# Performance work log

Hardware: AMD Instinct MI355X
Metric: run time of the kernel (lower is better)

Reference implementation:

```python
import jax, jax.numpy as jnp
import numpy as np

N = 5000          # nodes (pool_ratios = [2000/5000, 0.5])
KS = (2000, 1000, 500)  # top-k sizes per level, depth=3
H = 128           # inter_dim
IN = 3            # xyz
OUT = 6890        # SMPL template vertices
E = 80000


def _gcn(adj, x, W, b):
    # GCNConv: add self-loops (weight 1), symmetric normalization
    n = adj.shape[0]
    A = adj + jnp.eye(n, dtype=adj.dtype)
    dinv = jax.lax.rsqrt(A.sum(axis=1))
    Ahat = dinv[:, None] * A * dinv[None, :]
    return Ahat @ (x @ W) + b


def _augment(adj):
    # GraphUNet.augment_adj: remove self loops, add self loops, A @ A, remove self loops
    n = adj.shape[0]
    eye = jnp.eye(n, dtype=adj.dtype)
    A = adj * (1.0 - eye) + eye
    A2 = A @ A
    return A2 * (1.0 - eye)


def _pool(x, adj, w, k):
    # TopKPooling: score = tanh(x.w / ||w||), keep top-k, scale kept features by score
    score = jnp.tanh((x @ w) / jnp.linalg.norm(w))
    sc, perm = jax.lax.top_k(score, k)
    x = x[perm] * sc[:, None]
    adj = adj[perm][:, perm]
    return x, adj, perm


def reference(pos, edge_index, Wd0, bd0, Wd1, bd1, Wd2, bd2, Wd3, bd3,
              pw0, pw1, pw2, Wu0, bu0, Wu1, bu1, Wu2, bu2,
              W1, b1, W2, b2, W3, b3):
    # eval mode: dropout_adj(p=0.1, training=False) is identity
    adj = jnp.zeros((N, N), pos.dtype).at[edge_index[0], edge_index[1]].add(1.0)

    x = jax.nn.relu(_gcn(adj, pos, Wd0, bd0))
    xs, adjs, perms = [x], [adj], []
    Wds = [(Wd1, bd1), (Wd2, bd2), (Wd3, bd3)]
    pws = [pw0, pw1, pw2]

    adj_cur = adj
    for i in range(3):
        a = _augment(adj_cur)
        x, adj_cur, perm = _pool(x, a, pws[i], KS[i])
        Wi, bi = Wds[i]
        x = jax.nn.relu(_gcn(adj_cur, x, Wi, bi))
        if i < 2:
            xs.append(x)
            adjs.append(adj_cur)
        perms.append(perm)

    Wus = [(Wu0, bu0), (Wu1, bu1), (Wu2, bu2)]
    for i in range(3):
        j = 2 - i
        res = xs[j]
        up = jnp.zeros_like(res).at[perms[j]].set(x)  # unpool: scatter back
        x = res + up                                   # sum_res=True
        Wi, bi = Wus[i]
        x = _gcn(adjs[j], x, Wi, bi)
        if i < 2:
            x = jax.nn.relu(x)

    x = x @ W1 + b1
    x = jax.nn.relu(x) @ W2 + b2
    x = x @ W3 + b3
    return jax.nn.log_softmax(x, axis=1)


def _glorot(k, shape):
    return (jax.random.normal(k, shape) * np.sqrt(2.0 / (shape[0] + shape[1]))).astype(jnp.float32)


def setup_inputs() -> dict:
    key = jax.random.key(0)
    ks = jax.random.split(key, 16)
    inp = {
        'pos': jax.random.normal(ks[0], (N, IN), dtype=jnp.float32),
        'edge_index': jax.random.randint(ks[1], (2, E), 0, N, dtype=jnp.int64),
        'Wd0': _glorot(ks[2], (IN, H)), 'bd0': jnp.zeros((H,), jnp.float32),
        'Wd1': _glorot(ks[3], (H, H)), 'bd1': jnp.zeros((H,), jnp.float32),
        'Wd2': _glorot(ks[4], (H, H)), 'bd2': jnp.zeros((H,), jnp.float32),
        'Wd3': _glorot(ks[5], (H, H)), 'bd3': jnp.zeros((H,), jnp.float32),
        'pw0': jax.random.normal(ks[6], (H,), dtype=jnp.float32) / np.sqrt(H),
        'pw1': jax.random.normal(ks[7], (H,), dtype=jnp.float32) / np.sqrt(H),
        'pw2': jax.random.normal(ks[8], (H,), dtype=jnp.float32) / np.sqrt(H),
        'Wu0': _glorot(ks[9], (H, H)), 'bu0': jnp.zeros((H,), jnp.float32),
        'Wu1': _glorot(ks[10], (H, H)), 'bu1': jnp.zeros((H,), jnp.float32),
        'Wu2': _glorot(ks[11], (H, H)), 'bu2': jnp.zeros((H,), jnp.float32),
        'W1': _glorot(ks[12], (H, H)), 'b1': jnp.zeros((H,), jnp.float32),
        'W2': _glorot(ks[13], (H, H)), 'b2': jnp.zeros((H,), jnp.float32),
        'W3': _glorot(ks[14], (H, OUT)), 'b3': jnp.zeros((OUT,), jnp.float32),
    }
    return inp
```

## Files before the change

### kernel.cpp

```cpp
#include <hip/hip_runtime.h>
#include <cmath>

#define CDIV(a,b) (((a)+(b)-1)/(b))

using u16 = unsigned short;
using short8 = __attribute__((ext_vector_type(8))) short;
using f32x4 = __attribute__((ext_vector_type(4))) float;

__device__ __forceinline__ u16 f2b(float v) {
    union { float f; unsigned u; } x; x.f = v;
    unsigned r = x.u + 0x7fffu + ((x.u >> 16) & 1u);
    return (u16)(r >> 16);
}
__device__ __forceinline__ float b2f(u16 h) {
    union { unsigned u; float f; } x; x.u = ((unsigned)h) << 16;
    return x.f;
}

#if defined(__has_builtin)
#if __has_builtin(__builtin_amdgcn_global_load_lds)
#define HAS_GLL 1
#endif
#endif
#ifndef HAS_GLL
#define HAS_GLL 0
#endif

__device__ __forceinline__ void g2l(const u16* g, uint4* l) {
#if HAS_GLL
    __builtin_amdgcn_global_load_lds((const __attribute__((address_space(1))) void*)g,
                                     (__attribute__((address_space(3))) void*)l, 16, 0, 0);
#else
    *l = *(const uint4*)g;
#endif
}


__global__ void csr_cnt_k(const int* __restrict__ ei, int E, int* __restrict__ rowcnt) {
    int e = blockIdx.x * 256 + threadIdx.x;
    if (e < E) atomicAdd(&rowcnt[ei[e]], 1);
}

__global__ __launch_bounds__(1024) void prefix_k(const int* __restrict__ cnt, int* __restrict__ ptr, int n) {
    __shared__ int buf[5120];
    for (int i = threadIdx.x; i < 5120; i += 1024) buf[i] = (i < n) ? cnt[i] : 0;
    __syncthreads();
    for (int d = 1; d < 5120; d <<= 1) {
        int vals[5];
#pragma unroll
        for (int c = 0; c < 5; ++c) {
            int i = threadIdx.x + c * 1024;
            vals[c] = (i >= d) ? buf[i - d] : 0;
        }
        __syncthreads();
#pragma unroll
        for (int c = 0; c < 5; ++c) {
            int i = threadIdx.x + c * 1024;
            buf[i] += vals[c];
        }
        __syncthreads();
    }
    for (int i = threadIdx.x; i <= n; i += 1024) ptr[i] = (i == 0) ? 0 : buf[i - 1];
}

__global__ void csr_fill_k(const int* __restrict__ ei, int E, const int* __restrict__ rowptr,
                           int* __restrict__ fill, int* __restrict__ cols) {
    int e = blockIdx.x * 256 + threadIdx.x;
    if (e < E) {
        int u = ei[e];
        int p = rowptr[u] + atomicAdd(&fill[u], 1);
        cols[p] = ei[E + e];
    }
}

__global__ void sortrows_k(const int* __restrict__ rowptr, int* __restrict__ cols, int n) {
    int i = blockIdx.x * 256 + threadIdx.x;
    if (i >= n) return;
    int s = rowptr[i], e = rowptr[i + 1];
    for (int p = s + 1; p < e; ++p) {
        int v = cols[p];
        int q = p - 1;
        while (q >= s && cols[q] > v) { cols[q + 1] = cols[q]; --q; }
        cols[q + 1] = v;
    }
}

__global__ void dinv_from_cnt_k(const int* __restrict__ cnt, float* __restrict__ dinv, int n) {
    int i = blockIdx.x * 256 + threadIdx.x;
    if (i < n) dinv[i] = rsqrtf((float)cnt[i] + 1.0f);
}

__global__ __launch_bounds__(128) void spmm_gcn_k(const int* __restrict__ rowptr, const int* __restrict__ cols,
                                                  const float* __restrict__ dinv, const float* __restrict__ xw,
                                                  const float* __restrict__ bias, float* __restrict__ y, int relu) {
    int i = blockIdx.x, f = threadIdx.x;
    int s = rowptr[i], e = rowptr[i + 1];
    float acc = 0.f;
    for (int p = s; p < e; ++p) {
        int d = cols[p];
        acc += dinv[d] * xw[(size_t)d * 128 + f];
    }
    float di = dinv[i];
    float v = di * acc + di * di * xw[(size_t)i * 128 + f] + bias[f];
    y[(size_t)i * 128 + f] = relu ? fmaxf(v, 0.f) : v;
}


__global__ void inv_k(const int* __restrict__ perm, int k, int* __restrict__ inv) {
    int r = blockIdx.x * 256 + threadIdx.x;
    if (r < k) inv[perm[r]] = r;
}

__global__ __launch_bounds__(256) void spgemm_k(const int* __restrict__ perm, const int* __restrict__ rowptr,
                                                const int* __restrict__ cols, const int* __restrict__ inv,
                                                int* __restrict__ A2, int ldo) {
    __shared__ int nb[256];
    __shared__ int degs;
    int a = blockIdx.x;
    int pa = perm[a];
    int s = rowptr[pa], epos = rowptr[pa + 1];
    int d = epos - s;
    if (threadIdx.x == 0) degs = d > 256 ? 256 : d;
    if (threadIdx.x < d && threadIdx.x < 256) nb[threadIdx.x] = cols[s + threadIdx.x];
    __syncthreads();
    int* rowA2 = A2 + (size_t)a * ldo;
    for (int p = s + threadIdx.x; p < epos; p += 256) {
        int c = cols[p];
        if (c != pa) {
            int b = inv[c];
            if (b >= 0) atomicAdd(&rowA2[b], 2);
        }
    }
    int dd = degs;
    for (int j = 0; j < dd; ++j) {
        int kk = nb[j];
        if (kk == pa) continue;
        int s2 = rowptr[kk], e2 = rowptr[kk + 1];
        for (int p = s2 + threadIdx.x; p < e2; p += 256) {
            int pb = cols[p];
            if (pb != kk) {
                int b = inv[pb];
                if (b >= 0) atomicAdd(&rowA2[b], 1);
            }
        }
    }
}

__global__ void conv_spg_k(const int* __restrict__ A2, int kNew, int Mp, u16* __restrict__ out) {
    int r = blockIdx.x;
    for (int j = threadIdx.x; j < Mp; j += 256) {
        int v = 0;
        if (r < kNew && j < kNew && j != r) v = A2[(size_t)r * Mp + j];
        out[(size_t)r * Mp + j] = f2b((float)v);
    }
}


__global__ void rowsum_dinv_b_k(const u16* __restrict__ adjb, int ld, int n, float* __restrict__ dinv) {
    int i = blockIdx.x;
    __shared__ float red[256];
    const u16* row = adjb + (size_t)i * ld;
    float s = 0.f;
    for (int j = threadIdx.x; j < n; j += 256) s += b2f(row[j]);
    red[threadIdx.x] = s; __syncthreads();
    for (int w = 128; w > 0; w >>= 1) {
        if (threadIdx.x < w) red[threadIdx.x] += red[threadIdx.x + w];
        __syncthreads();
    }
    if (threadIdx.x == 0) dinv[i] = rsqrtf(red[0] + 1.0f);
}

__global__ void transpose_b_k(const u16* __restrict__ in, u16* __restrict__ out, int n) {
    __shared__ u16 t[64][65];
    int i0 = blockIdx.y * 64, j0 = blockIdx.x * 64;
    for (int e = threadIdx.x; e < 4096; e += 256) {
        int r = e >> 6, c = e & 63;
        t[r][c] = in[(size_t)(i0 + r) * n + j0 + c];
    }
    __syncthreads();
    for (int e = threadIdx.x; e < 4096; e += 256) {
        int r = e >> 6, c = e & 63;
        out[(size_t)(j0 + r) * n + i0 + c] = t[c][r];
    }
}


template<int SA, int SB>
__global__ __launch_bounds__(256) void mm_nt(const u16* __restrict__ A0, const u16* __restrict__ A1,
                                             const u16* __restrict__ B0, const u16* __restrict__ B1,
                                             float* __restrict__ C, const float* __restrict__ cbias,
                                             int M, int N, int lda, int ldb, int ldc,
                                             int kPerZ, int Kpad, size_t cstride) {
    __shared__ uint4 lds_t[(2 + SA + SB) * 512];
    uint4* Ab  = lds_t;
    uint4* A1b = lds_t + (SA ? 512 : 0);
    uint4* Bb  = lds_t + (1 + SA) * 512;
    uint4* B1b = Bb + (SB ? 512 : 0);

    int tid = threadIdx.x;

    int nx = gridDim.x, nxy = nx * gridDim.y;
    int bx = blockIdx.x, by = blockIdx.y;
    if ((nxy & 7) == 0) {
        int flat = by * nx + bx;
        int nf = (flat & 7) * (nxy >> 3) + (flat >> 3);
        bx = nf % nx; by = nf / nx;
    }
    int row0 = by * 128, col0 = bx * 128;

    int kbeg = blockIdx.z * kPerZ;
    int kend = min(kbeg + kPerZ, Kpad);
    C += (size_t)blockIdx.z * cstride;

    int wave = tid >> 6, lane = tid & 63;
    int wr = (wave >> 1) * 64, wc = (wave & 1) * 64;
    int lrow = lane & 15, kg = lane >> 4;

    int tS0 = tid, tS1 = tid + 256;
    int R0 = ((tS0 >> 6) << 4) | (tS0 & 15), kc0 = (tS0 >> 4) & 3;
    int R1 = ((tS1 >> 6) << 4) | (tS1 & 15), kc1 = (tS1 >> 4) & 3;

    const u16* aP0 = A0 + (size_t)(row0 + R0) * lda + kbeg + kc0 * 8;
    const u16* aP1 = A0 + (size_t)(row0 + R1) * lda + kbeg + kc1 * 8;
    const u16* bP0 = B0 + (size_t)(col0 + R0) * ldb + kbeg + kc0 * 8;
    const u16* bP1 = B0 + (size_t)(col0 + R1) * ldb + kbeg + kc1 * 8;
    const u16* a1P0 = SA ? (A1 + (size_t)(row0 + R0) * lda + kbeg + kc0 * 8) : nullptr;
    const u16* a1P1 = SA ? (A1 + (size_t)(row0 + R1) * lda + kbeg + kc1 * 8) : nullptr;
    const u16* b1P0 = SB ? (B1 + (size_t)(col0 + R0) * ldb + kbeg + kc0 * 8) : nullptr;
    const u16* b1P1 = SB ? (B1 + (size_t)(col0 + R1) * ldb + kbeg + kc1 * 8) : nullptr;

    f32x4 acc[4][4] = {};

    for (int k0 = kbeg; k0 < kend; k0 += 32) {
        __syncthreads();
        g2l(aP0, Ab + tS0);
        g2l(aP1, Ab + tS1);
        if constexpr (SA) { g2l(a1P0, A1b + tS0); g2l(a1P1, A1b + tS1); }
        g2l(bP0, Bb + tS0);
        g2l(bP1, Bb + tS1);
        if constexpr (SB) { g2l(b1P0, B1b + tS0); g2l(b1P1, B1b + tS1); }
        __syncthreads();

        const short8* Ap  = (const short8*)Ab;
        const short8* A1p = (const short8*)A1b;
        const short8* Bp  = (const short8*)Bb;
        const short8* B1p = (const short8*)B1b;

        short8 a[4], a1[4], b[4], b1[4];
#pragma unroll
        for (int m = 0; m < 4; ++m) {
            int idx = (((wr >> 4) + m) << 6) | (kg << 4) | lrow;
            a[m] = Ap[idx];
            if constexpr (SA) a1[m] = A1p[idx];
        }
#pragma unroll
        for (int n = 0; n < 4; ++n) {
            int idx = (((wc >> 4) + n) << 6) | (kg << 4) | lrow;
            b[n] = Bp[idx];
            if constexpr (SB) b1[n] = B1p[idx];
        }
#pragma unroll
        for (int m = 0; m < 4; ++m)
#pragma unroll
            for (int n = 0; n < 4; ++n) {
                acc[m][n] = __builtin_amdgcn_mfma_f32_16x16x32_bf16(a[m], b[n], acc[m][n], 0, 0, 0);
                if constexpr (SA) acc[m][n] = __builtin_amdgcn_mfma_f32_16x16x32_bf16(a1[m], b[n], acc[m][n], 0, 0, 0);
                if constexpr (SB) acc[m][n] = __builtin_amdgcn_mfma_f32_16x16x32_bf16(a[m], b1[n], acc[m][n], 0, 0, 0);
            }

        aP0 += 32; aP1 += 32; bP0 += 32; bP1 += 32;
        if constexpr (SA) { a1P0 += 32; a1P1 += 32; }
        if constexpr (SB) { b1P0 += 32; b1P1 += 32; }
    }

#pragma unroll
    for (int m = 0; m < 4; ++m) {
        int rm = row0 + wr + m * 16 + kg * 4;
#pragma unroll
        for (int n = 0; n < 4; ++n) {
            int cc = col0 + wc + n * 16 + lrow;
            if (cc >= N) continue;
            float badd = cbias ? cbias[cc] : 0.f;
#pragma unroll
            for (int i = 0; i < 4; ++i) {
                int r = rm + i;
                if (r < M) C[(size_t)r * ldc + cc] = acc[m][n][i] + badd;
            }
        }
    }
}


__global__ __launch_bounds__(256) void gemm64(const float* __restrict__ A, const float* __restrict__ B,
                                              float* __restrict__ C,
                                              int M, int N, int K, int lda, int ldb, int ldc,
                                              const float* __restrict__ bias, int relu) {
    __shared__ float As[16][65];
    __shared__ float Bs[16][65];
    int tid = threadIdx.x;
    int trow = tid / 16, tcol = tid % 16;
    int row0 = blockIdx.y * 64 + trow * 4;
    int col0 = blockIdx.x * 64 + tcol * 4;
    float acc[4][4] = {};
    int am = tid >> 2;
    int ak = (tid & 3) * 4;
    int bk = tid >> 4;
    int bn = (tid & 15) * 4;
    for (int k0 = 0; k0 < K; k0 += 16) {
        int gm = blockIdx.y * 64 + am;
#pragma unroll
        for (int u = 0; u < 4; ++u) {
            int gk = k0 + ak + u;
            As[ak + u][am] = (gm < M && gk < K) ? A[(size_t)gm * lda + gk] : 0.f;
        }
        int gbk = k0 + bk;
#pragma unroll
        for (int u = 0; u < 4; ++u) {
            int gn = blockIdx.x * 64 + bn + u;
            Bs[bk][bn + u] = (gbk < K && gn < N) ? B[(size_t)gbk * ldb + gn] : 0.f;
        }
        __syncthreads();
#pragma unroll
        for (int kk = 0; kk < 16; ++kk) {
            float a[4], b[4];
#pragma unroll
            for (int i = 0; i < 4; ++i) a[i] = As[kk][trow * 4 + i];
#pragma unroll
            for (int j = 0; j < 4; ++j) b[j] = Bs[kk][tcol * 4 + j];
#pragma unroll
            for (int i = 0; i < 4; ++i)
#pragma unroll
                for (int j = 0; j < 4; ++j) acc[i][j] += a[i] * b[j];
        }
        __syncthreads();
    }
#pragma unroll
    for (int i = 0; i < 4; ++i) {
        int r = row0 + i;
        if (r >= M) continue;
#pragma unroll
        for (int j = 0; j < 4; ++j) {
            int c = col0 + j;
            if (c < N) {
                float v = acc[i][j] + (bias ? bias[c] : 0.f);
                if (relu) v = fmaxf(v, 0.f);
                C[(size_t)r * ldc + c] = v;
            }
        }
    }
}


__global__ void scale_split_k(const float* __restrict__ xw, const float* __restrict__ dinv,
                              u16* __restrict__ zhT, u16* __restrict__ zlT, int M, int ldz) {
    __shared__ float t[32][33];
    int i0 = blockIdx.x * 32, f0 = blockIdx.y * 32;
#pragma unroll
    for (int it = 0; it < 4; ++it) {
        int r = it * 8 + (threadIdx.x >> 5);
        int c = threadIdx.x & 31;
        int i = i0 + r;
        t[r][c] = (i < M) ? dinv[i] * xw[(size_t)i * 128 + f0 + c] : 0.f;
    }
    __syncthreads();
#pragma unroll
    for (int it = 0; it < 4; ++it) {
        int r = it * 8 + (threadIdx.x >> 5);
        int c = threadIdx.x & 31;
        int f = f0 + r, i = i0 + c;
        float v = t[c][r];
        u16 h = f2b(v);
        zhT[(size_t)f * ldz + i] = h;
        zlT[(size_t)f * ldz + i] = f2b(v - b2f(h));
    }
}

__global__ void reduce_gcn_post_k(const float* __restrict__ part, int Z, int Mp,
                                  const float* __restrict__ xw, const float* __restrict__ dinv,
                                  const float* __restrict__ bias, float* __restrict__ y, int relu) {
    int i = blockIdx.x, f = threadIdx.x;
    size_t idx = (size_t)i * 128 + f;
    float s = 0.f;
    for (int z = 0; z < Z; ++z) s += part[(size_t)z * Mp * 128 + idx];
    float di = dinv[i];
    float v = di * s + di * di * xw[idx] + bias[f];
    y[idx] = relu ? fmaxf(v, 0.f) : v;
}


__global__ void score_k(const float* __restrict__ x, const float* __restrict__ pw,
                        float* __restrict__ score) {
    int i = blockIdx.x;
    __shared__ float red[128], red2[128];
    float p = pw[threadIdx.x];
    red[threadIdx.x]  = x[(size_t)i * 128 + threadIdx.x] * p;
    red2[threadIdx.x] = p * p;
    __syncthreads();
    for (int s = 64; s > 0; s >>= 1) {
        if (threadIdx.x < s) { red[threadIdx.x] += red[threadIdx.x + s]; red2[threadIdx.x] += red2[threadIdx.x + s]; }
        __syncthreads();
    }
    if (threadIdx.x == 0) score[i] = tanhf(red[0] / sqrtf(red2[0]));
}

__global__ __launch_bounds__(256) void rank_partial_k(const float* __restrict__ score, int n,
                                                      int* __restrict__ rankpart) {
    __shared__ float s_sh[512];
    int i = blockIdx.x * 256 + threadIdx.x;
    int jbase = blockIdx.y * 512;
    float si = (i < n) ? score[i] : -3.0f;
    for (int t = threadIdx.x; t < 512; t += 256) {
        int j = jbase + t;
        s_sh[t] = (j < n) ? score[j] : -3.0f;
    }
    __syncthreads();
    int cnt = 0;
#pragma unroll 16
    for (int t = 0; t < 512; ++t) {
        float sj = s_sh[t];
        cnt += (sj > si) || (sj == si && (jbase + t) < i);
    }
    if (i < n) rankpart[blockIdx.y * n + i] = cnt;
}

__global__ void scatter_topk_k(const float* __restrict__ score, const int* __restrict__ rankpart,
                               int nsl, int n, int k, int* __restrict__ perm, float* __restrict__ sc) {
    int i = blockIdx.x * 256 + threadIdx.x;
    if (i >= n) return;
    int r = 0;
    for (int s = 0; s < nsl; ++s) r += rankpart[s * n + i];
    if (r < k) { perm[r] = i; sc[r] = score[i]; }
}

__global__ void pool_x_k(float* __restrict__ xo, const float* __restrict__ xi,
                         const int* __restrict__ perm, const float* __restrict__ sc) {
    int a = blockIdx.x, f = threadIdx.x;
    xo[(size_t)a * 128 + f] = xi[(size_t)perm[a] * 128 + f] * sc[a];
}

__global__ void gather2_b_k(const u16* __restrict__ src0, const u16* __restrict__ src1,
                            int ldsrc, const int* __restrict__ perm,
                            u16* __restrict__ dst0, u16* __restrict__ dst1, int width) {
    const u16* src = blockIdx.y ? src1 : src0;
    u16* dst = blockIdx.y ? dst1 : dst0;
    int row = blockIdx.x;
    int p = perm[row];
    const uint4* s4 = (const uint4*)(src + (size_t)p * ldsrc);
    uint4* d4 = (uint4*)(dst + (size_t)row * width);
    int n8 = width >> 3;
    for (int j = threadIdx.x; j < n8; j += 256) d4[j] = s4[j];
    __syncthreads();
    if (threadIdx.x == 0) dst[(size_t)row * width + p] = 0x3F80;
}

__global__ void reduce_pool_k(const float* __restrict__ part, int Z, int k, int Mp, u16* __restrict__ out) {
    int row = blockIdx.x;
    for (int j = threadIdx.x; j < Mp; j += 256) {
        float s = 0.f;
        if (row < k && j < k) {
            for (int z = 0; z < Z; ++z) s += part[(size_t)z * Mp * Mp + (size_t)row * Mp + j];
            if (j == row) s = 0.f;
        }
        out[(size_t)row * Mp + j] = f2b(s);
    }
}

__global__ void scatter_add_k(float* __restrict__ xdst, const int* __restrict__ perm,
                              const float* __restrict__ xsrc) {
    int a = blockIdx.x, f = threadIdx.x;
    xdst[(size_t)perm[a] * 128 + f] += xsrc[(size_t)a * 128 + f];
}


__global__ void split_head_k(const float* __restrict__ x, u16* __restrict__ Ah, u16* __restrict__ Al) {
    int i = blockIdx.x, f = threadIdx.x;
    size_t idx = (size_t)i * 128 + f;
    float v = x[idx];
    u16 h = f2b(v);
    Ah[idx] = h;
    Al[idx] = f2b(v - b2f(h));
}

__global__ void convW3T_k(const float* __restrict__ W3, u16* __restrict__ W3T, int Nc, int Ncp) {
    __shared__ float t[64][65];
    int k0 = blockIdx.y * 64, n0 = blockIdx.x * 64;
    for (int e = threadIdx.x; e < 4096; e += 256) {
        int r = e >> 6, c = e & 63;
        t[r][c] = (k0 + r < 128 && n0 + c < Nc) ? W3[(size_t)(k0 + r) * Nc + n0 + c] : 0.f;
    }
    __syncthreads();
    for (int e = threadIdx.x; e < 4096; e += 256) {
        int r = e >> 6, c = e & 63;
        int nn = n0 + r, kk = k0 + c;
        if (nn < Ncp) W3T[(size_t)nn * 128 + kk] = f2b(t[c][r]);
    }
}

__global__ __launch_bounds__(256) void logsoftmax_k(float* __restrict__ out) {
    const int C = 6890;
    const int CPT = 27;
    int row = blockIdx.x;
    float* rowp = out + (size_t)row * C;
    __shared__ float red[256];

    float v[CPT];
    float mx = -1e30f;
#pragma unroll
    for (int u = 0; u < CPT; ++u) {
        int c = threadIdx.x + u * 256;
        v[u] = (c < C) ? rowp[c] : -1e30f;
        mx = fmaxf(mx, v[u]);
    }
    red[threadIdx.x] = mx; __syncthreads();
    for (int s = 128; s > 0; s >>= 1) {
        if (threadIdx.x < s) red[threadIdx.x] = fmaxf(red[threadIdx.x], red[threadIdx.x + s]);
        __syncthreads();
    }
    float m = red[0];
    __syncthreads();

    float sum = 0.f;
#pragma unroll
    for (int u = 0; u < CPT; ++u) sum += __expf(v[u] - m);
    red[threadIdx.x] = sum; __syncthreads();
    for (int s = 128; s > 0; s >>= 1) {
        if (threadIdx.x < s) red[threadIdx.x] += red[threadIdx.x + s];
        __syncthreads();
    }
    float ls = m + logf(red[0]);

#pragma unroll
    for (int u = 0; u < CPT; ++u) {
        int c = threadIdx.x + u * 256;
        if (c < C) rowp[c] = v[u] - ls;
    }
}


extern "C" void kernel_launch(void* const* d_in, const int* in_sizes, int n_in,
                              void* d_out, int out_size, void* d_ws, size_t ws_size,
                              hipStream_t stream) {
    const int N0 = 5000, K1 = 2000, K2 = 1000, K3 = 500, E = 80000, OUTC = 6890;
    const int Kp1 = 2048, Kp2 = 1024, Kp3 = 512, OUTCP = 6912;
    (void)in_sizes; (void)n_in; (void)out_size; (void)ws_size;

    const float* pos = (const float*)d_in[0];
    const int*   ei  = (const int*)d_in[1];
    const float* Wd0 = (const float*)d_in[2];  const float* bd0 = (const float*)d_in[3];
    const float* Wd1 = (const float*)d_in[4];  const float* bd1 = (const float*)d_in[5];
    const float* Wd2 = (const float*)d_in[6];  const float* bd2 = (const float*)d_in[7];
    const float* Wd3 = (const float*)d_in[8];  const float* bd3 = (const float*)d_in[9];
    const float* pw0 = (const float*)d_in[10];
    const float* pw1 = (const float*)d_in[11];
    const float* pw2 = (const float*)d_in[12];
    const float* Wu0 = (const float*)d_in[13]; const float* bu0 = (const float*)d_in[14];
    const float* Wu1 = (const float*)d_in[15]; const float* bu1 = (const float*)d_in[16];
    const float* Wu2 = (const float*)d_in[17]; const float* bu2 = (const float*)d_in[18];
    const float* W1  = (const float*)d_in[19]; const float* b1  = (const float*)d_in[20];
    const float* W2  = (const float*)d_in[21]; const float* b2  = (const float*)d_in[22];
    const float* W3  = (const float*)d_in[23]; const float* b3  = (const float*)d_in[24];

    float* w = (float*)d_ws;
    size_t off = 0;
    auto alloc = [&](size_t nel) { float* p = w + off; off += nel; return p; };

    float* pool = alloc(26220000);
    float* partials = pool;
    u16* G   = (u16*)(pool + 13000000);
    u16* HT  = (u16*)(pool + 18250000);
    u16* zhT = (u16*)(pool + 13000000);
    u16* zlT = (u16*)(pool + 13400000);
    u16* Ah  = (u16*)(pool);
    u16* Al  = (u16*)(pool + 400000);

    u16* adj1b  = (u16*)alloc(2097152);
    u16* adj1bT = (u16*)alloc(2097152);
    u16* adj2b  = (u16*)alloc(524288);
    u16* adj2bT = (u16*)alloc(524288);
    u16* adj3b  = (u16*)alloc(131072);
    u16* W3T    = (u16*)alloc(442368);

    float* x0 = alloc((size_t)N0 * 128);
    float* x1 = alloc((size_t)K1 * 128);
    float* x2 = alloc((size_t)K2 * 128);
    float* xa = alloc((size_t)N0 * 128);
    float* xb = alloc((size_t)N0 * 128);
    float* xw = alloc((size_t)N0 * 128);
    float* dinv0 = alloc(N0); float* dinv1 = alloc(K1); float* dinv2 = alloc(K2); float* dinv3 = alloc(K3);
    float* scorev = alloc(N0);
    float* scv    = alloc(K1);
    int* perm0 = (int*)alloc(K1);
    int* perm1 = (int*)alloc(K2);
    int* perm2 = (int*)alloc(K3);
    int* rankpart = (int*)alloc(50048);
    int* rowcnt = (int*)alloc(5120);
    int* rowptr = (int*)alloc(5120);
    int* fillc  = (int*)alloc(5120);
    int* colsb  = (int*)alloc(80000);
    int* invb   = (int*)alloc(5120);

    auto launch_mm = [&](int SA, int SB, const u16* A0, const u16* A1, const u16* B0, const u16* B1,
                         float* Cc, const float* cbias, int M, int N, int Kpad,
                         int lda, int ldb, int ldc, size_t cstride, int Z) -> int {
        int kPerZ = CDIV(Kpad, Z * 32) * 32;
        int gz = CDIV(Kpad, kPerZ);
        dim3 g(CDIV(N, 128), CDIV(M, 128), gz);
        if (SA)      mm_nt<1, 0><<<g, 256, 0, stream>>>(A0, A1, B0, B1, Cc, cbias, M, N, lda, ldb, ldc, kPerZ, Kpad, cstride);
        else if (SB) mm_nt<0, 1><<<g, 256, 0, stream>>>(A0, A1, B0, B1, Cc, cbias, M, N, lda, ldb, ldc, kPerZ, Kpad, cstride);
        else         mm_nt<0, 0><<<g, 256, 0, stream>>>(A0, A1, B0, B1, Cc, cbias, M, N, lda, ldb, ldc, kPerZ, Kpad, cstride);
        return gz;
    };

    auto run_gcn = [&](const u16* adjb, int n, int Np,
                       const float* x, const float* W, const float* bias,
                       const float* dinv, int relu, float* y, int Z) {
        gemm64<<<dim3(2, CDIV(n, 64)), 256, 0, stream>>>(x, W, xw, n, 128, 128, 128, 128, 128, nullptr, 0);
        scale_split_k<<<dim3(Np / 32, 4), 256, 0, stream>>>(xw, dinv, zhT, zlT, n, Np);
        int gz = launch_mm(0, 1, adjb, nullptr, zhT, zlT, partials, nullptr,
                           Np, 128, Np, Np, Np, 128, (size_t)Np * 128, Z);
        reduce_gcn_post_k<<<n, 128, 0, stream>>>(partials, gz, Np, xw, dinv, bias, y, relu);
    };

    auto run_gcn_sp = [&](const float* x, int kin, const float* W, const float* bias, int relu, float* y) {
        gemm64<<<dim3(2, CDIV(N0, 64)), 256, 0, stream>>>(x, W, xw, N0, 128, kin, kin, 128, 128, nullptr, 0);
        spmm_gcn_k<<<N0, 128, 0, stream>>>(rowptr, colsb, dinv0, xw, bias, y, relu);
    };

    auto run_pool = [&](const float* x, int n, int Np, int kNew, int KpNew, const float* pw,
                        const u16* srcb, const u16* srcbT, u16* adjNew, int* perm, int Z) {
        score_k<<<n, 128, 0, stream>>>(x, pw, scorev);
        int nsl = CDIV(n, 512);
        rank_partial_k<<<dim3(CDIV(n, 256), nsl), 256, 0, stream>>>(scorev, n, rankpart);
        scatter_topk_k<<<CDIV(n, 256), 256, 0, stream>>>(scorev, rankpart, nsl, n, kNew, perm, scv);
        pool_x_k<<<kNew, 128, 0, stream>>>(xa, x, perm, scv);
        gather2_b_k<<<dim3(kNew, 2), 256, 0, stream>>>(srcb, srcbT, Np, perm, G, HT, Np);
        int gz = launch_mm(0, 0, G, nullptr, HT, nullptr, partials, nullptr,
                           KpNew, KpNew, Np, Np, Np, KpNew, (size_t)KpNew * KpNew, Z);
        reduce_pool_k<<<KpNew, 256, 0, stream>>>(partials, gz, kNew, KpNew, adjNew);
    };

    hipMemsetAsync(rowcnt, 0, N0 * sizeof(int), stream);
    hipMemsetAsync(fillc, 0, N0 * sizeof(int), stream);
    csr_cnt_k<<<CDIV(E, 256), 256, 0, stream>>>(ei, E, rowcnt);
    prefix_k<<<1, 1024, 0, stream>>>(rowcnt, rowptr, N0);
    csr_fill_k<<<CDIV(E, 256), 256, 0, stream>>>(ei, E, rowptr, fillc, colsb);
    sortrows_k<<<CDIV(N0, 256), 256, 0, stream>>>(rowptr, colsb, N0);
    dinv_from_cnt_k<<<CDIV(N0, 256), 256, 0, stream>>>(rowcnt, dinv0, N0);

    run_gcn_sp(pos, 3, Wd0, bd0, 1, x0);

    score_k<<<N0, 128, 0, stream>>>(x0, pw0, scorev);
    {
        int nsl = CDIV(N0, 512);
        rank_partial_k<<<dim3(CDIV(N0, 256), nsl), 256, 0, stream>>>(scorev, N0, rankpart);
        scatter_topk_k<<<CDIV(N0, 256), 256, 0, stream>>>(scorev, rankpart, nsl, N0, K1, perm0, scv);
    }
    pool_x_k<<<K1, 128, 0, stream>>>(xa, x0, perm0, scv);
    hipMemsetAsync(invb, 0xFF, N0 * sizeof(int), stream);
    inv_k<<<CDIV(K1, 256), 256, 0, stream>>>(perm0, K1, invb);
    int* A2i = (int*)partials;
    hipMemsetAsync(A2i, 0, (size_t)Kp1 * Kp1 * sizeof(int), stream);
    spgemm_k<<<K1, 256, 0, stream>>>(perm0, rowptr, colsb, invb, A2i, Kp1);
    conv_spg_k<<<Kp1, 256, 0, stream>>>(A2i, K1, Kp1, adj1b);

    transpose_b_k<<<dim3(Kp1 / 64, Kp1 / 64), 256, 0, stream>>>(adj1b, adj1bT, Kp1);
    rowsum_dinv_b_k<<<K1, 256, 0, stream>>>(adj1b, Kp1, Kp1, dinv1);
    run_gcn(adj1b, K1, Kp1, xa, Wd1, bd1, dinv1, 1, x1, 16);

    run_pool(x1, K1, Kp1, K2, Kp2, pw1, adj1b, adj1bT, adj2b, perm1, 8);
    transpose_b_k<<<dim3(Kp2 / 64, Kp2 / 64), 256, 0, stream>>>(adj2b, adj2bT, Kp2);
    rowsum_dinv_b_k<<<K2, 256, 0, stream>>>(adj2b, Kp2, Kp2, dinv2);
    run_gcn(adj2b, K2, Kp2, xa, Wd2, bd2, dinv2, 1, x2, 16);

    run_pool(x2, K2, Kp2, K3, Kp3, pw2, adj2b, adj2bT, adj3b, perm2, 8);
    rowsum_dinv_b_k<<<K3, 256, 0, stream>>>(adj3b, Kp3, Kp3, dinv3);
    run_gcn(adj3b, K3, Kp3, xa, Wd3, bd3, dinv3, 1, xb, 8);

    hipMemcpyAsync(xa, x2, (size_t)K2 * 128 * sizeof(float), hipMemcpyDeviceToDevice, stream);
    scatter_add_k<<<K3, 128, 0, stream>>>(xa, perm2, xb);
    run_gcn(adj2b, K2, Kp2, xa, Wu0, bu0, dinv2, 1, xb, 16);

    hipMemcpyAsync(xa, x1, (size_t)K1 * 128 * sizeof(float), hipMemcpyDeviceToDevice, stream);
    scatter_add_k<<<K2, 128, 0, stream>>>(xa, perm1, xb);
    run_gcn(adj1b, K1, Kp1, xa, Wu1, bu1, dinv1, 1, xb, 16);

    hipMemcpyAsync(xa, x0, (size_t)N0 * 128 * sizeof(float), hipMemcpyDeviceToDevice, stream);
    scatter_add_k<<<K1, 128, 0, stream>>>(xa, perm0, xb);
    run_gcn_sp(xa, 128, Wu2, bu2, 0, xb);

    gemm64<<<dim3(2, CDIV(N0, 64)), 256, 0, stream>>>(xb, W1, xa, N0, 128, 128, 128, 128, 128, b1, 1);
    gemm64<<<dim3(2, CDIV(N0, 64)), 256, 0, stream>>>(xa, W2, xw, N0, 128, 128, 128, 128, 128, b2, 0);

    split_head_k<<<N0, 128, 0, stream>>>(xw, Ah, Al);
    convW3T_k<<<dim3(OUTCP / 64, 2), 256, 0, stream>>>(W3, W3T, OUTC, OUTCP);

    float* outp = (float*)d_out;
    launch_mm(1, 0, Ah, Al, W3T, nullptr, outp, b3, N0, OUTC, 128, 128, 128, OUTC, 0, 1);
    logsoftmax_k<<<N0, 256, 0, stream>>>(outp);
}
```

Measured before the change: 725.9 us.

## Use sparse CSR for level-1 GCN and fuse transposes into conversion kernels

Builds a weighted CSR (counts, prefix, fill) from the integer A² matrix at level 1 and runs the level-1 down and up GCNs as sparse SpMM instead of dense bf16 matmuls. The bf16 conversion and reduce-pool kernels now write the transposed copy directly, which removes the separate transpose launches. This avoids dense O(K1²) GEMM work on a sparse 2000×2000 adjacency. It adds extra CSR-building kernels and large cols/vals buffers, and the SpMM's per-row serial loop could be slow if A² rows are fairly dense (average degree ~1000+).

Measured after the change: 783.1 us. 7.9% more time.

```diff
diff --git a/kernel.cpp b/kernel.cpp
--- a/kernel.cpp
+++ b/kernel.cpp
@@ -99,6 +99,22 @@
     for (int p = s; p < e; ++p) {
         int d = cols[p];
         acc += dinv[d] * xw[(size_t)d * 128 + f];
+    }
+    float di = dinv[i];
+    float v = di * acc + di * di * xw[(size_t)i * 128 + f] + bias[f];
+    y[(size_t)i * 128 + f] = relu ? fmaxf(v, 0.f) : v;
+}
+
+__global__ __launch_bounds__(128) void spmm_gcn_v_k(const int* __restrict__ rowptr, const int* __restrict__ cols,
+                                                    const float* __restrict__ vals, const float* __restrict__ dinv,
+                                                    const float* __restrict__ xw, const float* __restrict__ bias,
+                                                    float* __restrict__ y, int relu) {
+    int i = blockIdx.x, f = threadIdx.x;
+    int s = rowptr[i], e = rowptr[i + 1];
+    float acc = 0.f;
+    for (int p = s; p < e; ++p) {
+        int d = cols[p];
+        acc += vals[p] * dinv[d] * xw[(size_t)d * 128 + f];
     }
     float di = dinv[i];
     float v = di * acc + di * di * xw[(size_t)i * 128 + f] + bias[f];
@@ -146,12 +162,66 @@
     }
 }
 
-__global__ void conv_spg_k(const int* __restrict__ A2, int kNew, int Mp, u16* __restrict__ out) {
+__global__ void conv_spgT_k(const int* __restrict__ A2, int kNew, int Mp,
+                            u16* __restrict__ out, u16* __restrict__ outT) {
+    __shared__ u16 t[64][65];
+    int i0 = blockIdx.y * 64, j0 = blockIdx.x * 64;
+    for (int e = threadIdx.x; e < 4096; e += 256) {
+        int r = e >> 6, c = e & 63;
+        int gi = i0 + r, gj = j0 + c;
+        int v = 0;
+        if (gi < kNew && gj < kNew && gi != gj) v = A2[(size_t)gi * Mp + gj];
+        u16 b = f2b((float)v);
+        out[(size_t)gi * Mp + gj] = b;
+        t[r][c] = b;
+    }
+    __syncthreads();
+    for (int e = threadIdx.x; e < 4096; e += 256) {
+        int r = e >> 6, c = e & 63;
+        outT[(size_t)(j0 + r) * Mp + i0 + c] = t[c][r];
+    }
+}
+
+__global__ __launch_bounds__(256) void cnt1_k(const int* __restrict__ A2, int k, int Mp,
+                                              int* __restrict__ rowcnt, float* __restrict__ dinv) {
     int r = blockIdx.x;
-    for (int j = threadIdx.x; j < Mp; j += 256) {
-        int v = 0;
-        if (r < kNew && j < kNew && j != r) v = A2[(size_t)r * Mp + j];
-        out[(size_t)r * Mp + j] = f2b((float)v);
+    __shared__ int redc[256], reds[256];
+    const int* row = A2 + (size_t)r * Mp;
+    int cnt = 0, sum = 0;
+    for (int j = threadIdx.x; j < k; j += 256) {
+        int v = row[j];
+        if (v != 0 && j != r) { ++cnt; sum += v; }
+    }
+    redc[threadIdx.x] = cnt; reds[threadIdx.x] = sum; __syncthreads();
+    for (int w = 128; w > 0; w >>= 1) {
+        if (threadIdx.x < w) { redc[threadIdx.x] += redc[threadIdx.x + w]; reds[threadIdx.x] += reds[threadIdx.x + w]; }
+        __syncthreads();
+    }
+    if (threadIdx.x == 0) { rowcnt[r] = redc[0]; dinv[r] = rsqrtf((float)reds[0] + 1.0f); }
+}
+
+__global__ __launch_bounds__(256) void fill1_k(const int* __restrict__ A2, int k, int Mp,
+                                               const int* __restrict__ rowptr,
+                                               int* __restrict__ cols, float* __restrict__ vals) {
+    int r = blockIdx.x;
+    __shared__ int base[256];
+    const int* row = A2 + (size_t)r * Mp;
+    int cnt = 0;
+    for (int j = threadIdx.x; j < k; j += 256) {
+        int v = row[j];
+        cnt += (v != 0 && j != r);
+    }
+    base[threadIdx.x] = cnt; __syncthreads();
+    for (int d = 1; d < 256; d <<= 1) {
+        int v = (threadIdx.x >= d) ? base[threadIdx.x - d] : 0;
+        __syncthreads();
+        base[threadIdx.x] += v;
+        __syncthreads();
+    }
+    int me = base[threadIdx.x] - cnt + rowptr[r];
+    for (int j = threadIdx.x; j < k; j += 256) {
+        int v = row[j];
+        if (v != 0 && j != r) { cols[me] = j; vals[me] = (float)v; ++me; }
     }
 }
 
@@ -168,20 +238,6 @@
         __syncthreads();
     }
     if (threadIdx.x == 0) dinv[i] = rsqrtf(red[0] + 1.0f);
-}
-
-__global__ void transpose_b_k(const u16* __restrict__ in, u16* __restrict__ out, int n) {
-    __shared__ u16 t[64][65];
-    int i0 = blockIdx.y * 64, j0 = blockIdx.x * 64;
-    for (int e = threadIdx.x; e < 4096; e += 256) {
-        int r = e >> 6, c = e & 63;
-        t[r][c] = in[(size_t)(i0 + r) * n + j0 + c];
-    }
-    __syncthreads();
-    for (int e = threadIdx.x; e < 4096; e += 256) {
-        int r = e >> 6, c = e & 63;
-        out[(size_t)(j0 + r) * n + i0 + c] = t[c][r];
-    }
 }
 
 
@@ -451,6 +507,28 @@
     for (int j = threadIdx.x; j < n8; j += 256) d4[j] = s4[j];
     __syncthreads();
     if (threadIdx.x == 0) dst[(size_t)row * width + p] = 0x3F80;
+}
+
+__global__ void reduce_poolT_k(const float* __restrict__ part, int Z, int k, int Mp,
+                               u16* __restrict__ out, u16* __restrict__ outT) {
+    __shared__ u16 t[64][65];
+    int i0 = blockIdx.y * 64, j0 = blockIdx.x * 64;
+    for (int e = threadIdx.x; e < 4096; e += 256) {
+        int r = e >> 6, c = e & 63;
+        int gi = i0 + r, gj = j0 + c;
+        float s = 0.f;
+        if (gi < k && gj < k && gi != gj) {
+            for (int z = 0; z < Z; ++z) s += part[(size_t)z * Mp * Mp + (size_t)gi * Mp + gj];
+        }
+        u16 b = f2b(s);
+        out[(size_t)gi * Mp + gj] = b;
+        t[r][c] = b;
+    }
+    __syncthreads();
+    for (int e = threadIdx.x; e < 4096; e += 256) {
+        int r = e >> 6, c = e & 63;
+        outT[(size_t)(j0 + r) * Mp + i0 + c] = t[c][r];
+    }
 }
 
 __global__ void reduce_pool_k(const float* __restrict__ part, int Z, int k, int Mp, u16* __restrict__ out) {
@@ -598,6 +676,10 @@
     int* fillc  = (int*)alloc(5120);
     int* colsb  = (int*)alloc(80000);
     int* invb   = (int*)alloc(5120);
+    int* rowcnt1 = (int*)alloc(2048);
+    int* rowptr1 = (int*)alloc(2080);
+    int* cols1   = (int*)alloc(4200000);
+    float* vals1 = alloc(4200000);
 
     auto launch_mm = [&](int SA, int SB, const u16* A0, const u16* A1, const u16* B0, const u16* B1,
                          float* Cc, const float* cbias, int M, int N, int Kpad,
@@ -626,17 +708,21 @@
         spmm_gcn_k<<<N0, 128, 0, stream>>>(rowptr, colsb, dinv0, xw, bias, y, relu);
     };
 
+    auto run_gcn_sp1 = [&](const float* x, const float* W, const float* bias, int relu, float* y) {
+        gemm64<<<dim3(2, CDIV(K1, 64)), 256, 0, stream>>>(x, W, xw, K1, 128, 128, 128, 128, 128, nullptr, 0);
+        spmm_gcn_v_k<<<K1, 128, 0, stream>>>(rowptr1, cols1, vals1, dinv1, xw, bias, y, relu);
+    };
+
     auto run_pool = [&](const float* x, int n, int Np, int kNew, int KpNew, const float* pw,
-                        const u16* srcb, const u16* srcbT, u16* adjNew, int* perm, int Z) {
+                        const u16* srcb, const u16* srcbT, int* perm, int Z) -> int {
         score_k<<<n, 128, 0, stream>>>(x, pw, scorev);
         int nsl = CDIV(n, 512);
         rank_partial_k<<<dim3(CDIV(n, 256), nsl), 256, 0, stream>>>(scorev, n, rankpart);
         scatter_topk_k<<<CDIV(n, 256), 256, 0, stream>>>(scorev, rankpart, nsl, n, kNew, perm, scv);
         pool_x_k<<<kNew, 128, 0, stream>>>(xa, x, perm, scv);
         gather2_b_k<<<dim3(kNew, 2), 256, 0, stream>>>(srcb, srcbT, Np, perm, G, HT, Np);
-        int gz = launch_mm(0, 0, G, nullptr, HT, nullptr, partials, nullptr,
-                           KpNew, KpNew, Np, Np, Np, KpNew, (size_t)KpNew * KpNew, Z);
-        reduce_pool_k<<<KpNew, 256, 0, stream>>>(partials, gz, kNew, KpNew, adjNew);
+        return launch_mm(0, 0, G, nullptr, HT, nullptr, partials, nullptr,
+                         KpNew, KpNew, Np, Np, Np, KpNew, (size_t)KpNew * KpNew, Z);
     };
 
     hipMemsetAsync(rowcnt, 0, N0 * sizeof(int), stream);
@@ -661,18 +747,24 @@
     int* A2i = (int*)partials;
     hipMemsetAsync(A2i, 0, (size_t)Kp1 * Kp1 * sizeof(int), stream);
     spgemm_k<<<K1, 256, 0, stream>>>(perm0, rowptr, colsb, invb, A2i, Kp1);
-    conv_spg_k<<<Kp1, 256, 0, stream>>>(A2i, K1, Kp1, adj1b);
-
-    transpose_b_k<<<dim3(Kp1 / 64, Kp1 / 64), 256, 0, stream>>>(adj1b, adj1bT, Kp1);
-    rowsum_dinv_b_k<<<K1, 256, 0, stream>>>(adj1b, Kp1, Kp1, dinv1);
-    run_gcn(adj1b, K1, Kp1, xa, Wd1, bd1, dinv1, 1, x1, 16);
-
-    run_pool(x1, K1, Kp1, K2, Kp2, pw1, adj1b, adj1bT, adj2b, perm1, 8);
-    transpose_b_k<<<dim3(Kp2 / 64, Kp2 / 64), 256, 0, stream>>>(adj2b, adj2bT, Kp2);
+    conv_spgT_k<<<dim3(Kp1 / 64, Kp1 / 64), 256, 0, stream>>>(A2i, K1, Kp1, adj1b, adj1bT);
+    cnt1_k<<<K1, 256, 0, stream>>>(A2i, K1, Kp1, rowcnt1, dinv1);
+    prefix_k<<<1, 1024, 0, stream>>>(rowcnt1, rowptr1, K1);
+    fill1_k<<<K1, 256, 0, stream>>>(A2i, K1, Kp1, rowptr1, cols1, vals1);
+
+    run_gcn_sp1(xa, Wd1, bd1, 1, x1);
+
+    {
+        int gz = run_pool(x1, K1, Kp1, K2, Kp2, pw1, adj1b, adj1bT, perm1, 8);
+        reduce_poolT_k<<<dim3(Kp2 / 64, Kp2 / 64), 256, 0, stream>>>(partials, gz, K2, Kp2, adj2b, adj2bT);
+    }
     rowsum_dinv_b_k<<<K2, 256, 0, stream>>>(adj2b, Kp2, Kp2, dinv2);
     run_gcn(adj2b, K2, Kp2, xa, Wd2, bd2, dinv2, 1, x2, 16);
 
-    run_pool(x2, K2, Kp2, K3, Kp3, pw2, adj2b, adj2bT, adj3b, perm2, 8);
+    {
+        int gz = run_pool(x2, K2, Kp2, K3, Kp3, pw2, adj2b, adj2bT, perm2, 8);
+        reduce_pool_k<<<Kp3, 256, 0, stream>>>(partials, gz, K3, Kp3, adj3b);
+    }
     rowsum_dinv_b_k<<<K3, 256, 0, stream>>>(adj3b, Kp3, Kp3, dinv3);
     run_gcn(adj3b, K3, Kp3, xa, Wd3, bd3, dinv3, 1, xb, 8);
 
@@ -682,7 +774,7 @@
 
     hipMemcpyAsync(xa, x1, (size_t)K1 * 128 * sizeof(float), hipMemcpyDeviceToDevice, stream);
     scatter_add_k<<<K2, 128, 0, stream>>>(xa, perm1, xb);
-    run_gcn(adj1b, K1, Kp1, xa, Wu1, bu1, dinv1, 1, xb, 16);
+    run_gcn_sp1(xa, Wu1, bu1, 1, xb);
 
     hipMemcpyAsync(xa, x0, (size_t)N0 * 128 * sizeof(float), hipMemcpyDeviceToDevice, stream);
     scatter_add_k<<<K1, 128, 0, stream>>>(xa, perm0, xb);
```
